# Performance work log

Measured on AMD Instinct MI355X. Metric: run time of the kernel, lower is better.

The kernel has to match this reference:

```python
import jax, jax.numpy as jnp
import numpy as np

N = 10000      # nodes per QA graph
E = 128000     # edges per QA graph
A = 5          # answers (multiple choice)
D = 300        # glove embedding dim
H = 8          # heads layer 1
C1 = 64        # per-head out channels layer 1 (concat -> 512)
HID = 512
NEG_SLOPE = 0.2
EPS = 1e-16


def gat_layer(x, edge_index, W, a_src, a_dst, bias, concat):
    # x: [N, Din]; edge_index: [2, E]; W: [Din, H*C]; a_src/a_dst: [H, C]
    Hh, C = a_src.shape
    h = (x @ W).reshape(N, Hh, C)                      # transformed node feats
    alpha_src = (h * a_src[None]).sum(-1)              # [N, H]
    alpha_dst = (h * a_dst[None]).sum(-1)              # [N, H]
    src, dst = edge_index[0], edge_index[1]
    e = jax.nn.leaky_relu(alpha_src[src] + alpha_dst[dst], NEG_SLOPE)  # [E, H]
    # edge softmax grouped by destination node
    m = jax.ops.segment_max(e, dst, num_segments=N)    # [N, H]
    ex = jnp.exp(e - m[dst])
    denom = jax.ops.segment_sum(ex, dst, num_segments=N)
    alpha = ex / (denom[dst] + EPS)                    # [E, H]
    msg = alpha[:, :, None] * h[src]                   # [E, H, C]
    out = jax.ops.segment_sum(msg, dst, num_segments=N)  # [N, H, C]
    out = out.reshape(N, Hh * C) if concat else out.mean(axis=1)
    return out + bias, alpha


def setup_inputs() -> dict:
    key = jax.random.key(0)
    ks = jax.random.split(key, 10)
    s = 0.05
    return {
        "x": jax.random.normal(ks[0], (A, N, D), jnp.float32),
        "edge_index": jax.random.randint(ks[1], (A, 2, E), 0, N, dtype=jnp.int32),
        "W1": jax.random.normal(ks[2], (D, H * C1), jnp.float32) * s,
        "att_src1": jax.random.normal(ks[3], (H, C1), jnp.float32) * s,
        "att_dst1": jax.random.normal(ks[4], (H, C1), jnp.float32) * s,
        "bias1": jnp.zeros((H * C1,), jnp.float32),
        "W2": jax.random.normal(ks[5], (HID, 1), jnp.float32) * s,
        "att_src2": jax.random.normal(ks[6], (1, 1), jnp.float32) * s,
        "att_dst2": jax.random.normal(ks[7], (1, 1), jnp.float32) * s,
        "bias2": jnp.zeros((1,), jnp.float32),
    }


def reference(x, edge_index, W1, att_src1, att_dst1, bias1, W2, att_src2, att_dst2, bias2):
    def per_answer(xa, ei):
        h1, _ = gat_layer(xa, ei, W1, att_src1, att_dst1, bias1, concat=True)
        h1 = jax.nn.relu(h1)
        h2, alpha = gat_layer(h1, ei, W2, att_src2, att_dst2, bias2, concat=False)
        proba = h2.mean()                                  # scalar (x.mean(dim=0))
        # aggregate_attention: attention[dst] += edge_weight (edge_additive)
        att = jax.ops.segment_sum(alpha[:, 0], ei[1], num_segments=N)
        return proba, att

    proba_vec, atts = jax.vmap(per_answer)(x, edge_index)  # [A], [A, N]
    sel = atts[jnp.argmax(proba_vec)]                      # attentions[argmax]
    return proba_vec, sel
```

## Files before the change

### kernel.cpp

```cpp
#include <hip/hip_runtime.h>
#include <hip/hip_bf16.h>
#include <math.h>

#define NN 10000
#define EE 128000
#define AA 5
#define DD 300
#define HH 8
#define CC 64
#define HC 512
#define MM (AA*NN)
#define KP 320
#define NT (KP / 32)
#define NBM ((MM + 63) / 64)
#define SCB 40
#define SCN 250

typedef __attribute__((ext_vector_type(8))) _Float16 f16x8;
typedef __attribute__((ext_vector_type(4))) float f32x4;
typedef __attribute__((ext_vector_type(2))) float f32x2;
typedef unsigned short ushort;
typedef unsigned char uchar;

__device__ __forceinline__ ushort f2bf(float f) {
    unsigned u = __float_as_uint(f);
    unsigned r = u + 0x7fffu + ((u >> 16) & 1u);
    return (ushort)(r >> 16);
}
__device__ __forceinline__ float bf2f(ushort h) {
    return __uint_as_float(((unsigned)h) << 16);
}


__global__ void zero_cnt(int* cnt) {
    int i = blockIdx.x * 256 + threadIdx.x;
    if (i < AA * NN) cnt[i] = 0;
}

__global__ void count_edges(const int* __restrict__ ei, int* __restrict__ cnt) {
    int a = blockIdx.y;
    int e = blockIdx.x * 256 + threadIdx.x;
    if (e < EE) {
        int dst = ei[(size_t)a * 2 * EE + EE + e];
        atomicAdd(&cnt[a * NN + dst], 1);
    }
}


__global__ __launch_bounds__(256) void scan_bsum(const int* __restrict__ cnt,
                                                 int* __restrict__ bsum) {
    int a = blockIdx.y, b = blockIdx.x;
    int l = threadIdx.x;
    int v = (l < SCN) ? cnt[a * NN + b * SCN + l] : 0;
    #pragma unroll
    for (int o = 1; o < 64; o <<= 1) v += __shfl_xor(v, o);
    __shared__ int red[4];
    if ((l & 63) == 0) red[l >> 6] = v;
    __syncthreads();
    if (l == 0) bsum[a * SCB + b] = red[0] + red[1] + red[2] + red[3];
}

__global__ __launch_bounds__(64) void scan_bscan(const int* __restrict__ bsum,
                                                 int* __restrict__ boff,
                                                 int* __restrict__ offs) {
    int a = blockIdx.x;
    int l = threadIdx.x;
    int v = (l < SCB) ? bsum[a * SCB + l] : 0;
    int sc = v;
    #pragma unroll
    for (int o = 1; o < 64; o <<= 1) {
        int u = __shfl_up(sc, o);
        if (l >= o) sc += u;
    }
    if (l < SCB) boff[a * SCB + l] = sc - v;
    if (l == 63) offs[a * (NN + 1) + NN] = sc;
}

__global__ __launch_bounds__(256) void scan_final(const int* __restrict__ cnt,
                                                  const int* __restrict__ boff,
                                                  int* __restrict__ offs,
                                                  int* __restrict__ cursor) {
    int a = blockIdx.y, b = blockIdx.x;
    int l = threadIdx.x;
    int i = b * SCN + l;
    int v = (l < SCN) ? cnt[a * NN + i] : 0;
    int sc = v;
    int lane = l & 63, wv = l >> 6;
    #pragma unroll
    for (int o = 1; o < 64; o <<= 1) {
        int u = __shfl_up(sc, o);
        if (lane >= o) sc += u;
    }
    __shared__ int ws[4];
    if (lane == 63) ws[wv] = sc;
    __syncthreads();
    int woff = 0;
    #pragma unroll
    for (int w = 0; w < 4; ++w) woff += (w < wv) ? ws[w] : 0;
    if (l < SCN) {
        int o = boff[a * SCB + b] + woff + sc - v;
        offs[a * (NN + 1) + i] = o;
        cursor[a * (NN + 1) + i] = o;
    }
}

__global__ void scatter_edges(const int* __restrict__ ei, int* __restrict__ cursor,
                              int* __restrict__ csr_eid) {
    int a = blockIdx.y;
    int e = blockIdx.x * 256 + threadIdx.x;
    if (e < EE) {
        int dst = ei[(size_t)a * 2 * EE + EE + e];
        int pos = atomicAdd(&cursor[a * (NN + 1) + dst], 1);
        csr_eid[(size_t)a * EE + pos] = e;
    }
}

__global__ __launch_bounds__(256) void sort_src(const int* __restrict__ ei,
                                                const int* __restrict__ offs,
                                                int* __restrict__ csr_eid,
                                                int* __restrict__ csr_src,
                                                int* __restrict__ csr_dst) {
    int a = blockIdx.y;
    int wid = threadIdx.x >> 6, l = threadIdx.x & 63;
    int n = blockIdx.x * 4 + wid;
    if (n >= NN) return;
    const int* offsA = offs + a * (NN + 1);
    int beg = offsA[n], end = offsA[n + 1];
    int deg = end - beg;
    int* seg = csr_eid + (size_t)a * EE + beg;
    const int* srcrow = ei + (size_t)a * 2 * EE;
    if (deg <= 64) {
        int v = (l < deg) ? seg[l] : 0x7fffffff;
        #pragma unroll
        for (int k = 2; k <= 64; k <<= 1)
            #pragma unroll
            for (int j = k >> 1; j > 0; j >>= 1) {
                int p = __shfl_xor(v, j);
                bool keepMin = (((l & k) == 0) == ((l & j) == 0));
                int mn = min(v, p), mx = max(v, p);
                v = keepMin ? mn : mx;
            }
        if (l < deg) {
            csr_src[(size_t)a * EE + beg + l] = srcrow[v];
            csr_dst[(size_t)a * EE + beg + l] = n;
        }
    } else {
        if (l == 0) {
            for (int i = 1; i < deg; ++i) {
                int key = seg[i];
                int j = i - 1;
                while (j >= 0 && seg[j] > key) { seg[j + 1] = seg[j]; --j; }
                seg[j + 1] = key;
            }
        }
        __builtin_amdgcn_wave_barrier();
        for (int i = l; i < deg; i += 64) {
            csr_src[(size_t)a * EE + beg + i] = srcrow[seg[i]];
            csr_dst[(size_t)a * EE + beg + i] = n;
        }
    }
}


__global__ __launch_bounds__(256) void pack_x(const float* __restrict__ X,
                                              ushort* __restrict__ Xp) {
    int gid = blockIdx.x * 256 + threadIdx.x;
    if (gid >= NBM * NT * 4 * 64) return;
    int l = gid & 63;
    int fr = (gid >> 6) & 3;
    int rest = gid >> 8;
    int ks = rest % NT;
    int bmi = rest / NT;
    int row = bmi * 64 + fr * 16 + (l & 15);
    int k = ks * 32 + (l >> 4) * 8;
    f16x8 o;
    if (row < MM && k + 8 <= DD) {
        float4 v0 = *(const float4*)(X + (size_t)row * DD + k);
        float4 v1 = *(const float4*)(X + (size_t)row * DD + k + 4);
        o[0] = (_Float16)v0.x; o[1] = (_Float16)v0.y;
        o[2] = (_Float16)v0.z; o[3] = (_Float16)v0.w;
        o[4] = (_Float16)v1.x; o[5] = (_Float16)v1.y;
        o[6] = (_Float16)v1.z; o[7] = (_Float16)v1.w;
    } else {
        #pragma unroll
        for (int j = 0; j < 8; ++j)
            o[j] = (row < MM && k + j < DD) ? (_Float16)X[(size_t)row * DD + k + j]
                                            : (_Float16)0.f;
    }
    *(f16x8*)(Xp + (size_t)gid * 8) = o;
}

__global__ __launch_bounds__(256) void pack_w(const float* __restrict__ W,
                                              ushort* __restrict__ Wp) {
    int gid = blockIdx.x * 256 + threadIdx.x;
    if (gid >= HH * NT * 4 * 64) return;
    int l = gid & 63;
    int fc = (gid >> 6) & 3;
    int rest = gid >> 8;
    int ks = rest % NT;
    int head = rest / NT;
    int col = head * 64 + fc * 16 + (l & 15);
    int k = ks * 32 + (l >> 4) * 8;
    f16x8 o;
    #pragma unroll
    for (int j = 0; j < 8; ++j)
        o[j] = (k + j < DD) ? (_Float16)W[(size_t)(k + j) * HC + col] : (_Float16)0.f;
    *(f16x8*)(Wp + (size_t)gid * 8) = o;
}


__global__ __launch_bounds__(256) void gemm_f16(const ushort* __restrict__ Xp,
                                                const ushort* __restrict__ Wp,
                                                const float* __restrict__ att_src1,
                                                const float* __restrict__ att_dst1,
                                                uchar* __restrict__ Hout,
                                                float* __restrict__ asrc,
                                                float* __restrict__ adst) {
    int wid = blockIdx.x * 4 + (threadIdx.x >> 6);
    int bmi = wid >> 3, head = wid & 7;
    if (bmi >= NBM) return;
    int bm = bmi * 64;
    int l = threadIdx.x & 63;
    int l16 = l & 15, kg = l >> 4;

    const ushort* Abase = Xp + (size_t)bmi * NT * 2048 + l * 8;
    const ushort* Bbase = Wp + (size_t)head * NT * 2048 + l * 8;

    f32x4 zz = {0.f, 0.f, 0.f, 0.f};
    f32x4 acc[4][4];
    #pragma unroll
    for (int i = 0; i < 4; ++i)
        #pragma unroll
        for (int j = 0; j < 4; ++j) acc[i][j] = zz;

    f16x8 aX[4], bX[4], aY[4], bY[4];
    #pragma unroll
    for (int f = 0; f < 4; ++f) {
        aX[f] = *(const f16x8*)(Abase + f * 512);
        bX[f] = *(const f16x8*)(Bbase + f * 512);
    }

    #pragma unroll
    for (int kk = 0; kk < NT; kk += 2) {
        if (kk + 1 < NT) {
            #pragma unroll
            for (int f = 0; f < 4; ++f) {
                aY[f] = *(const f16x8*)(Abase + (kk + 1) * 2048 + f * 512);
                bY[f] = *(const f16x8*)(Bbase + (kk + 1) * 2048 + f * 512);
            }
        }
        #pragma unroll
        for (int fr = 0; fr < 4; ++fr)
            #pragma unroll
            for (int fc = 0; fc < 4; ++fc)
                acc[fr][fc] = __builtin_amdgcn_mfma_f32_16x16x32_f16(aX[fr], bX[fc], acc[fr][fc], 0, 0, 0);
        if (kk + 2 < NT) {
            #pragma unroll
            for (int f = 0; f < 4; ++f) {
                aX[f] = *(const f16x8*)(Abase + (kk + 2) * 2048 + f * 512);
                bX[f] = *(const f16x8*)(Bbase + (kk + 2) * 2048 + f * 512);
            }
        }
        if (kk + 1 < NT) {
            #pragma unroll
            for (int fr = 0; fr < 4; ++fr)
                #pragma unroll
                for (int fc = 0; fc < 4; ++fc)
                    acc[fr][fc] = __builtin_amdgcn_mfma_f32_16x16x32_f16(aY[fr], bY[fc], acc[fr][fc], 0, 0, 0);
        }
    }

    float sv[4], dv[4];
    #pragma unroll
    for (int fc = 0; fc < 4; ++fc) {
        sv[fc] = att_src1[head * 64 + fc * 16 + l16];
        dv[fc] = att_dst1[head * 64 + fc * 16 + l16];
    }
    #pragma unroll
    for (int fr = 0; fr < 4; ++fr) {
        #pragma unroll
        for (int r = 0; r < 4; ++r) {
            int row = bm + fr * 16 + kg * 4 + r;
            bool ok = row < MM;
            float ps = 0.f, pd = 0.f;
            #pragma unroll
            for (int fc = 0; fc < 4; ++fc) {
                float val = acc[fr][fc][r];
                if (ok) {
                    int pk = __builtin_amdgcn_cvt_pk_fp8_f32(val, val, 0, false);
                    Hout[(size_t)row * HC + head * 64 + fc * 16 + l16] = (uchar)(pk & 0xff);
                }
                ps = fmaf(val, sv[fc], ps);
                pd = fmaf(val, dv[fc], pd);
            }
            #pragma unroll
            for (int o = 1; o < 16; o <<= 1) {
                ps += __shfl_xor(ps, o);
                pd += __shfl_xor(pd, o);
            }
            if (l16 == 0 && ok) {
                asrc[(size_t)row * HH + head] = ps;
                adst[(size_t)row * HH + head] = pd;
            }
        }
    }
}


__global__ __launch_bounds__(256) void edge_w(const int* __restrict__ csr_src,
                                              const int* __restrict__ csr_dst,
                                              const float* __restrict__ asrc,
                                              const float* __restrict__ adst,
                                              float* __restrict__ w4) {
    int a = blockIdx.y;
    int gid = blockIdx.x * 256 + threadIdx.x;
    if (gid >= EE * HH) return;
    int slot = gid >> 3, hd = gid & 7;
    int s = csr_src[(size_t)a * EE + slot];
    int d = csr_dst[(size_t)a * EE + slot];
    float v = asrc[((size_t)a * NN + s) * HH + hd] + adst[((size_t)a * NN + d) * HH + hd];
    v = v > 0.f ? v : 0.2f * v;
    w4[(((size_t)a * 2 + (hd >> 2)) * EE + slot) * 4 + (hd & 3)] = __expf(v);
}


__global__ __launch_bounds__(256) void layer1_agg(const uchar* __restrict__ h1,
                                                  const float* __restrict__ w4,
                                                  const int* __restrict__ offs,
                                                  const int* __restrict__ csr_src,
                                                  const float* __restrict__ bias1,
                                                  const float* __restrict__ W2,
                                                  float* __restrict__ h2p) {
    int a = blockIdx.y;
    int hf = blockIdx.z;
    int wid = threadIdx.x >> 6, l = threadIdx.x & 63;
    int n = blockIdx.x * 4 + wid;
    int l32 = l & 31;
    int ehalf = l >> 5;
    int hs = l32 >> 3;

    const int* offsA = offs + a * (NN + 1);
    int beg = offsA[n], end = offsA[n + 1];
    int deg = end - beg;
    const int* srcs = csr_src + (size_t)a * EE + beg;
    const float* wA = w4 + (((size_t)a * 2 + hf) * EE + beg) * 4;
    const uchar* h1A = h1 + (size_t)a * NN * HC + hf * 256;

    float denom = 0.f;
    float acc[8] = {};

    for (int c0 = 0; c0 < deg; c0 += 16) {
        int ei_w = c0 + (l >> 2);
        float w_reg = (ei_w < deg) ? wA[c0 * 4 + l] : 0.f;
        denom += w_reg;
        int s_reg = srcs[min(c0 + (l & 15), deg - 1)];
        #pragma unroll
        for (int j = 0; j < 16; j += 2) {
            int e = j + ehalf;
            float wj = __shfl(w_reg, e * 4 + hs);
            int sj = __shfl(s_reg, min(e, 15));
            const uchar* rp = h1A + (size_t)sj * HC + l32 * 8;
            uint2 hv = *(const uint2*)rp;
            f32x2 p0 = __builtin_amdgcn_cvt_pk_f32_fp8((int)hv.x, false);
            f32x2 p1 = __builtin_amdgcn_cvt_pk_f32_fp8((int)hv.x, true);
            f32x2 p2 = __builtin_amdgcn_cvt_pk_f32_fp8((int)hv.y, false);
            f32x2 p3 = __builtin_amdgcn_cvt_pk_f32_fp8((int)hv.y, true);
            acc[0] = fmaf(wj, p0[0], acc[0]);
            acc[1] = fmaf(wj, p0[1], acc[1]);
            acc[2] = fmaf(wj, p1[0], acc[2]);
            acc[3] = fmaf(wj, p1[1], acc[3]);
            acc[4] = fmaf(wj, p2[0], acc[4]);
            acc[5] = fmaf(wj, p2[1], acc[5]);
            acc[6] = fmaf(wj, p3[0], acc[6]);
            acc[7] = fmaf(wj, p3[1], acc[7]);
        }
    }
    #pragma unroll
    for (int k = 0; k < 8; ++k) acc[k] += __shfl_xor(acc[k], 32);
    #pragma unroll
    for (int o = 4; o < 64; o <<= 1) denom += __shfl_xor(denom, o);
    float dn = __shfl(denom, hs);
    float inv = 1.f / (dn + 1e-16f);

    int cb = hf * 256 + l32 * 8;
    float4 b0 = *(const float4*)(bias1 + cb);
    float4 b1 = *(const float4*)(bias1 + cb + 4);
    float4 w0 = *(const float4*)(W2 + cb);
    float4 w1 = *(const float4*)(W2 + cb + 4);
    float bz[8] = {b0.x, b0.y, b0.z, b0.w, b1.x, b1.y, b1.z, b1.w};
    float wz[8] = {w0.x, w0.y, w0.z, w0.w, w1.x, w1.y, w1.z, w1.w};
    float p = 0.f;
    #pragma unroll
    for (int k = 0; k < 8; ++k) {
        float z = fmaf(acc[k], inv, bz[k]);
        z = z > 0.f ? z : 0.f;
        p = fmaf(z, wz[k], p);
    }
    #pragma unroll
    for (int o = 1; o < 32; o <<= 1) p += __shfl_xor(p, o);
    if (l == 0) h2p[((size_t)hf * AA + a) * NN + n] = p;
}

__global__ void sum_h2(const float* __restrict__ h2p, float* __restrict__ h2) {
    int i = blockIdx.x * 256 + threadIdx.x;
    if (i < AA * NN) h2[i] = h2p[i] + h2p[(size_t)AA * NN + i];
}


#define L2GRID 40

__global__ __launch_bounds__(256) void layer2_proba(const float* __restrict__ h2,
                                                    const int* __restrict__ offs,
                                                    const int* __restrict__ csr_src,
                                                    const float* __restrict__ att_src2,
                                                    const float* __restrict__ att_dst2,
                                                    const float* __restrict__ bias2,
                                                    float* __restrict__ partials) {
    int a = blockIdx.y;
    int n = blockIdx.x * 256 + threadIdx.x;
    float out2 = 0.f;
    if (n < NN) {
        const int* offsA = offs + a * (NN + 1);
        const int* srcs = csr_src + (size_t)a * EE;
        const float* h2A = h2 + (size_t)a * NN;
        float as2 = att_src2[0], ad2 = att_dst2[0];
        int beg = offsA[n], end = offsA[n + 1];
        float adn = h2A[n] * ad2;
        float denom = 0.f, accv = 0.f;
        for (int i = beg; i < end; ++i) {
            float hs = h2A[srcs[i]];
            float v = fmaf(hs, as2, adn);
            v = v > 0.f ? v : 0.2f * v;
            float w = __expf(v);
            denom += w;
            accv = fmaf(w, hs, accv);
        }
        out2 = accv / (denom + 1e-16f) + bias2[0];
    }
    __shared__ float red[256];
    red[threadIdx.x] = out2;
    __syncthreads();
    for (int s = 128; s > 0; s >>= 1) {
        if (threadIdx.x < s) red[threadIdx.x] += red[threadIdx.x + s];
        __syncthreads();
    }
    if (threadIdx.x == 0) partials[a * L2GRID + blockIdx.x] = red[0];
}

__global__ __launch_bounds__(256) void finalize_proba(const float* __restrict__ partials,
                                                      float* __restrict__ out,
                                                      int* __restrict__ best) {
    int tid = threadIdx.x;
    __shared__ float red[256];
    red[tid] = (tid < AA * L2GRID) ? partials[tid] : 0.f;
    __syncthreads();
    if (tid == 0) {
        float pv[AA];
        for (int a = 0; a < AA; ++a) {
            float s = 0.f;
            for (int i = 0; i < L2GRID; ++i) s += red[a * L2GRID + i];
            pv[a] = s / (float)NN;
            out[a] = pv[a];
        }
        int b = 0;
        for (int a = 1; a < AA; ++a)
            if (pv[a] > pv[b]) b = a;
        *best = b;
    }
}

__global__ void write_sel(const int* __restrict__ cnt, const int* __restrict__ best,
                          float* __restrict__ out) {
    int n = blockIdx.x * 256 + threadIdx.x;
    if (n < NN) out[AA + n] = (cnt[(*best) * NN + n] > 0) ? 1.0f : 0.0f;
}


extern "C" void kernel_launch(void* const* d_in, const int* in_sizes, int n_in,
                              void* d_out, int out_size, void* d_ws, size_t ws_size,
                              hipStream_t stream) {
    const float* x        = (const float*)d_in[0];
    const int*   ei       = (const int*)d_in[1];
    const float* W1       = (const float*)d_in[2];
    const float* att_src1 = (const float*)d_in[3];
    const float* att_dst1 = (const float*)d_in[4];
    const float* bias1    = (const float*)d_in[5];
    const float* W2       = (const float*)d_in[6];
    const float* att_src2 = (const float*)d_in[7];
    const float* att_dst2 = (const float*)d_in[8];
    const float* bias2    = (const float*)d_in[9];
    float* out = (float*)d_out;

    char* ws = (char*)d_ws;
    size_t off = 0;
    auto alloc = [&](size_t bytes) {
        size_t cur = off;
        off += (bytes + 255) & ~(size_t)255;
        return cur;
    };
    uchar*  h1      = (uchar*)(ws + alloc(sizeof(uchar) * (size_t)MM * HC));
    ushort* xp      = (ushort*)(ws + alloc(sizeof(ushort) * (size_t)NBM * NT * 2048));
    float*  asrc    = (float*)(ws + alloc(sizeof(float) * (size_t)MM * HH));
    float*  adst    = (float*)(ws + alloc(sizeof(float) * (size_t)MM * HH));
    float*  h2      = (float*)(ws + alloc(sizeof(float) * (size_t)MM));
    float*  h2p     = (float*)(ws + alloc(sizeof(float) * 2 * (size_t)MM));
    int*    cnt     = (int*)(ws + alloc(sizeof(int) * (size_t)AA * NN));
    int*    offs    = (int*)(ws + alloc(sizeof(int) * (size_t)AA * (NN + 1)));
    int*    cursor  = (int*)(ws + alloc(sizeof(int) * (size_t)AA * (NN + 1)));
    int*    bsum    = (int*)(ws + alloc(sizeof(int) * (size_t)AA * SCB));
    int*    boff    = (int*)(ws + alloc(sizeof(int) * (size_t)AA * SCB));
    int*    csr_eid = (int*)(ws + alloc(sizeof(int) * (size_t)AA * EE));
    int*    csr_src = (int*)(ws + alloc(sizeof(int) * (size_t)AA * EE));
    int*    csr_dst = (int*)(ws + alloc(sizeof(int) * (size_t)AA * EE));
    float*  w4      = (float*)(ws + alloc(sizeof(float) * (size_t)AA * EE * HH));
    float*  partials= (float*)(ws + alloc(sizeof(float) * AA * L2GRID));
    int*    best    = (int*)(ws + alloc(sizeof(int) * 16));
    ushort* wp      = (ushort*)(ws + alloc(sizeof(ushort) * (size_t)HH * NT * 2048));
    (void)ws_size; (void)in_sizes; (void)n_in; (void)out_size;

    pack_w<<<dim3((HH * NT * 256 + 255) / 256), dim3(256), 0, stream>>>(W1, wp);
    pack_x<<<dim3((NBM * NT * 256 + 255) / 256), dim3(256), 0, stream>>>(x, xp);

    zero_cnt<<<dim3((AA * NN + 255) / 256), dim3(256), 0, stream>>>(cnt);
    count_edges<<<dim3(EE / 256, AA), dim3(256), 0, stream>>>(ei, cnt);
    scan_bsum<<<dim3(SCB, AA), dim3(256), 0, stream>>>(cnt, bsum);
    scan_bscan<<<dim3(AA), dim3(64), 0, stream>>>(bsum, boff, offs);
    scan_final<<<dim3(SCB, AA), dim3(256), 0, stream>>>(cnt, boff, offs, cursor);
    scatter_edges<<<dim3(EE / 256, AA), dim3(256), 0, stream>>>(ei, cursor, csr_eid);
    sort_src<<<dim3(NN / 4, AA), dim3(256), 0, stream>>>(ei, offs, csr_eid, csr_src, csr_dst);

    gemm_f16<<<dim3((NBM * 8 + 3) / 4), dim3(256), 0, stream>>>(
        xp, wp, att_src1, att_dst1, h1, asrc, adst);

    edge_w<<<dim3(EE * HH / 256, AA), dim3(256), 0, stream>>>(csr_src, csr_dst,
                                                              asrc, adst, w4);

    layer1_agg<<<dim3(NN / 4, AA, 2), dim3(256), 0, stream>>>(h1, w4, offs, csr_src,
                                                              bias1, W2, h2p);
    sum_h2<<<dim3((AA * NN + 255) / 256), dim3(256), 0, stream>>>(h2p, h2);

    layer2_proba<<<dim3(L2GRID, AA), dim3(256), 0, stream>>>(h2, offs, csr_src,
                                                             att_src2, att_dst2, bias2,
                                                             partials);

    finalize_proba<<<dim3(1), dim3(256), 0, stream>>>(partials, out, best);
    write_sel<<<dim3((NN + 255) / 256), dim3(256), 0, stream>>>(cnt, best, out);
}
```

Before: 244.0 us.

## Fuse edge weight computation into sort_src and merge layer1 aggregation halves

Moves the leaky-relu/exp edge-weight computation into the CSR sort kernel, which now runs after the GEMM. This removes the separate edge_w kernel and the csr_dst array. The layer-1 aggregation now handles all 512 channels per wavefront with 8 edges per step and prefetches the next batch of weights and sources. That removes the two-half grid and the sum_h2 reduction kernel. The trade-offs are less parallelism in aggregation and serialising the sort behind the GEMM.

```diff
diff --git a/kernel.cpp b/kernel.cpp
--- a/kernel.cpp
+++ b/kernel.cpp
@@ -30,6 +30,10 @@
 __device__ __forceinline__ float bf2f(ushort h) {
     return __uint_as_float(((unsigned)h) << 16);
 }
+__device__ __forceinline__ float leaky_exp(float v) {
+    v = v > 0.f ? v : 0.2f * v;
+    return __expf(v);
+}
 
 
 __global__ void zero_cnt(int* cnt) {
@@ -115,11 +119,14 @@
     }
 }
 
+
 __global__ __launch_bounds__(256) void sort_src(const int* __restrict__ ei,
                                                 const int* __restrict__ offs,
                                                 int* __restrict__ csr_eid,
                                                 int* __restrict__ csr_src,
-                                                int* __restrict__ csr_dst) {
+                                                const float* __restrict__ asrc,
+                                                const float* __restrict__ adst,
+                                                float* __restrict__ w_csr) {
     int a = blockIdx.y;
     int wid = threadIdx.x >> 6, l = threadIdx.x & 63;
     int n = blockIdx.x * 4 + wid;
@@ -129,6 +136,11 @@
     int deg = end - beg;
     int* seg = csr_eid + (size_t)a * EE + beg;
     const int* srcrow = ei + (size_t)a * 2 * EE;
+    const float* asrcA = asrc + (size_t)a * NN * HH;
+    const float* adstA = adst + (size_t)a * NN * HH;
+    float4 d0 = *(const float4*)(adstA + (size_t)n * HH);
+    float4 d1 = *(const float4*)(adstA + (size_t)n * HH + 4);
+
     if (deg <= 64) {
         int v = (l < deg) ? seg[l] : 0x7fffffff;
         #pragma unroll
@@ -141,8 +153,18 @@
                 v = keepMin ? mn : mx;
             }
         if (l < deg) {
-            csr_src[(size_t)a * EE + beg + l] = srcrow[v];
-            csr_dst[(size_t)a * EE + beg + l] = n;
+            int s = srcrow[v];
+            csr_src[(size_t)a * EE + beg + l] = s;
+            float4 s0 = *(const float4*)(asrcA + (size_t)s * HH);
+            float4 s1 = *(const float4*)(asrcA + (size_t)s * HH + 4);
+            float4 w0, w1;
+            w0.x = leaky_exp(s0.x + d0.x); w0.y = leaky_exp(s0.y + d0.y);
+            w0.z = leaky_exp(s0.z + d0.z); w0.w = leaky_exp(s0.w + d0.w);
+            w1.x = leaky_exp(s1.x + d1.x); w1.y = leaky_exp(s1.y + d1.y);
+            w1.z = leaky_exp(s1.z + d1.z); w1.w = leaky_exp(s1.w + d1.w);
+            float* wp = w_csr + ((size_t)a * EE + beg + l) * HH;
+            *(float4*)(wp) = w0;
+            *(float4*)(wp + 4) = w1;
         }
     } else {
         if (l == 0) {
@@ -155,8 +177,18 @@
         }
         __builtin_amdgcn_wave_barrier();
         for (int i = l; i < deg; i += 64) {
-            csr_src[(size_t)a * EE + beg + i] = srcrow[seg[i]];
-            csr_dst[(size_t)a * EE + beg + i] = n;
+            int s = srcrow[seg[i]];
+            csr_src[(size_t)a * EE + beg + i] = s;
+            float4 s0 = *(const float4*)(asrcA + (size_t)s * HH);
+            float4 s1 = *(const float4*)(asrcA + (size_t)s * HH + 4);
+            float4 w0, w1;
+            w0.x = leaky_exp(s0.x + d0.x); w0.y = leaky_exp(s0.y + d0.y);
+            w0.z = leaky_exp(s0.z + d0.z); w0.w = leaky_exp(s0.w + d0.w);
+            w1.x = leaky_exp(s1.x + d1.x); w1.y = leaky_exp(s1.y + d1.y);
+            w1.z = leaky_exp(s1.z + d1.z); w1.w = leaky_exp(s1.w + d1.w);
+            float* wp = w_csr + ((size_t)a * EE + beg + i) * HH;
+            *(float4*)(wp) = w0;
+            *(float4*)(wp + 4) = w1;
         }
     }
 }
@@ -307,82 +339,69 @@
 }
 
 
-__global__ __launch_bounds__(256) void edge_w(const int* __restrict__ csr_src,
-                                              const int* __restrict__ csr_dst,
-                                              const float* __restrict__ asrc,
-                                              const float* __restrict__ adst,
-                                              float* __restrict__ w4) {
-    int a = blockIdx.y;
-    int gid = blockIdx.x * 256 + threadIdx.x;
-    if (gid >= EE * HH) return;
-    int slot = gid >> 3, hd = gid & 7;
-    int s = csr_src[(size_t)a * EE + slot];
-    int d = csr_dst[(size_t)a * EE + slot];
-    float v = asrc[((size_t)a * NN + s) * HH + hd] + adst[((size_t)a * NN + d) * HH + hd];
-    v = v > 0.f ? v : 0.2f * v;
-    w4[(((size_t)a * 2 + (hd >> 2)) * EE + slot) * 4 + (hd & 3)] = __expf(v);
-}
-
-
 __global__ __launch_bounds__(256) void layer1_agg(const uchar* __restrict__ h1,
-                                                  const float* __restrict__ w4,
+                                                  const float* __restrict__ w_csr,
                                                   const int* __restrict__ offs,
                                                   const int* __restrict__ csr_src,
                                                   const float* __restrict__ bias1,
                                                   const float* __restrict__ W2,
-                                                  float* __restrict__ h2p) {
+                                                  float* __restrict__ h2) {
     int a = blockIdx.y;
-    int hf = blockIdx.z;
     int wid = threadIdx.x >> 6, l = threadIdx.x & 63;
     int n = blockIdx.x * 4 + wid;
-    int l32 = l & 31;
-    int ehalf = l >> 5;
-    int hs = l32 >> 3;
+    int eg = l >> 3;
+    int gh = l >> 3;
 
     const int* offsA = offs + a * (NN + 1);
     int beg = offsA[n], end = offsA[n + 1];
     int deg = end - beg;
     const int* srcs = csr_src + (size_t)a * EE + beg;
-    const float* wA = w4 + (((size_t)a * 2 + hf) * EE + beg) * 4;
-    const uchar* h1A = h1 + (size_t)a * NN * HC + hf * 256;
+    const float* wA = w_csr + ((size_t)a * EE + beg) * HH;
+    const uchar* h1A = h1 + (size_t)a * NN * HC;
 
     float denom = 0.f;
     float acc[8] = {};
 
-    for (int c0 = 0; c0 < deg; c0 += 16) {
-        int ei_w = c0 + (l >> 2);
-        float w_reg = (ei_w < deg) ? wA[c0 * 4 + l] : 0.f;
-        denom += w_reg;
-        int s_reg = srcs[min(c0 + (l & 15), deg - 1)];
+    float w_cur = (eg < deg) ? wA[l] : 0.f;
+    int s_cur = (eg < deg) ? srcs[eg] : 0;
+
+    for (int c0 = 0; c0 < deg; c0 += 8) {
+        float w_nxt = 0.f;
+        int s_nxt = 0;
+        if (c0 + 8 + eg < deg) {
+            w_nxt = wA[(c0 + 8) * 8 + l];
+            s_nxt = srcs[c0 + 8 + eg];
+        }
         #pragma unroll
-        for (int j = 0; j < 16; j += 2) {
-            int e = j + ehalf;
-            float wj = __shfl(w_reg, e * 4 + hs);
-            int sj = __shfl(s_reg, min(e, 15));
-            const uchar* rp = h1A + (size_t)sj * HC + l32 * 8;
-            uint2 hv = *(const uint2*)rp;
-            f32x2 p0 = __builtin_amdgcn_cvt_pk_f32_fp8((int)hv.x, false);
-            f32x2 p1 = __builtin_amdgcn_cvt_pk_f32_fp8((int)hv.x, true);
-            f32x2 p2 = __builtin_amdgcn_cvt_pk_f32_fp8((int)hv.y, false);
-            f32x2 p3 = __builtin_amdgcn_cvt_pk_f32_fp8((int)hv.y, true);
-            acc[0] = fmaf(wj, p0[0], acc[0]);
-            acc[1] = fmaf(wj, p0[1], acc[1]);
-            acc[2] = fmaf(wj, p1[0], acc[2]);
-            acc[3] = fmaf(wj, p1[1], acc[3]);
-            acc[4] = fmaf(wj, p2[0], acc[4]);
-            acc[5] = fmaf(wj, p2[1], acc[5]);
-            acc[6] = fmaf(wj, p3[0], acc[6]);
-            acc[7] = fmaf(wj, p3[1], acc[7]);
-        }
-    }
-    #pragma unroll
-    for (int k = 0; k < 8; ++k) acc[k] += __shfl_xor(acc[k], 32);
-    #pragma unroll
-    for (int o = 4; o < 64; o <<= 1) denom += __shfl_xor(denom, o);
-    float dn = __shfl(denom, hs);
+        for (int j = 0; j < 8; ++j) {
+            if (c0 + j < deg) {
+                float wj = __shfl(w_cur, j * 8 + gh);
+                int sj = __shfl(s_cur, j * 8);
+                uint2 hv = *(const uint2*)(h1A + (size_t)sj * HC + (l << 3));
+                f32x2 p0 = __builtin_amdgcn_cvt_pk_f32_fp8((int)hv.x, false);
+                f32x2 p1 = __builtin_amdgcn_cvt_pk_f32_fp8((int)hv.x, true);
+                f32x2 p2 = __builtin_amdgcn_cvt_pk_f32_fp8((int)hv.y, false);
+                f32x2 p3 = __builtin_amdgcn_cvt_pk_f32_fp8((int)hv.y, true);
+                acc[0] = fmaf(wj, p0[0], acc[0]);
+                acc[1] = fmaf(wj, p0[1], acc[1]);
+                acc[2] = fmaf(wj, p1[0], acc[2]);
+                acc[3] = fmaf(wj, p1[1], acc[3]);
+                acc[4] = fmaf(wj, p2[0], acc[4]);
+                acc[5] = fmaf(wj, p2[1], acc[5]);
+                acc[6] = fmaf(wj, p3[0], acc[6]);
+                acc[7] = fmaf(wj, p3[1], acc[7]);
+            }
+        }
+        denom += w_cur;
+        w_cur = w_nxt;
+        s_cur = s_nxt;
+    }
+    #pragma unroll
+    for (int o = 8; o < 64; o <<= 1) denom += __shfl_xor(denom, o);
+    float dn = __shfl(denom, gh);
     float inv = 1.f / (dn + 1e-16f);
 
-    int cb = hf * 256 + l32 * 8;
+    int cb = l * 8;
     float4 b0 = *(const float4*)(bias1 + cb);
     float4 b1 = *(const float4*)(bias1 + cb + 4);
     float4 w0 = *(const float4*)(W2 + cb);
@@ -397,13 +416,8 @@
         p = fmaf(z, wz[k], p);
     }
     #pragma unroll
-    for (int o = 1; o < 32; o <<= 1) p += __shfl_xor(p, o);
-    if (l == 0) h2p[((size_t)hf * AA + a) * NN + n] = p;
-}
-
-__global__ void sum_h2(const float* __restrict__ h2p, float* __restrict__ h2) {
-    int i = blockIdx.x * 256 + threadIdx.x;
-    if (i < AA * NN) h2[i] = h2p[i] + h2p[(size_t)AA * NN + i];
+    for (int o = 1; o < 64; o <<= 1) p += __shfl_xor(p, o);
+    if (l == 0) h2[(size_t)a * NN + n] = p;
 }
 
 
@@ -503,7 +517,6 @@
     float*  asrc    = (float*)(ws + alloc(sizeof(float) * (size_t)MM * HH));
     float*  adst    = (float*)(ws + alloc(sizeof(float) * (size_t)MM * HH));
     float*  h2      = (float*)(ws + alloc(sizeof(float) * (size_t)MM));
-    float*  h2p     = (float*)(ws + alloc(sizeof(float) * 2 * (size_t)MM));
     int*    cnt     = (int*)(ws + alloc(sizeof(int) * (size_t)AA * NN));
     int*    offs    = (int*)(ws + alloc(sizeof(int) * (size_t)AA * (NN + 1)));
     int*    cursor  = (int*)(ws + alloc(sizeof(int) * (size_t)AA * (NN + 1)));
@@ -511,8 +524,7 @@
     int*    boff    = (int*)(ws + alloc(sizeof(int) * (size_t)AA * SCB));
     int*    csr_eid = (int*)(ws + alloc(sizeof(int) * (size_t)AA * EE));
     int*    csr_src = (int*)(ws + alloc(sizeof(int) * (size_t)AA * EE));
-    int*    csr_dst = (int*)(ws + alloc(sizeof(int) * (size_t)AA * EE));
-    float*  w4      = (float*)(ws + alloc(sizeof(float) * (size_t)AA * EE * HH));
+    float*  w_csr   = (float*)(ws + alloc(sizeof(float) * (size_t)AA * EE * HH));
     float*  partials= (float*)(ws + alloc(sizeof(float) * AA * L2GRID));
     int*    best    = (int*)(ws + alloc(sizeof(int) * 16));
     ushort* wp      = (ushort*)(ws + alloc(sizeof(ushort) * (size_t)HH * NT * 2048));
@@ -527,17 +539,15 @@
     scan_bscan<<<dim3(AA), dim3(64), 0, stream>>>(bsum, boff, offs);
     scan_final<<<dim3(SCB, AA), dim3(256), 0, stream>>>(cnt, boff, offs, cursor);
     scatter_edges<<<dim3(EE / 256, AA), dim3(256), 0, stream>>>(ei, cursor, csr_eid);
-    sort_src<<<dim3(NN / 4, AA), dim3(256), 0, stream>>>(ei, offs, csr_eid, csr_src, csr_dst);
 
     gemm_f16<<<dim3((NBM * 8 + 3) / 4), dim3(256), 0, stream>>>(
         xp, wp, att_src1, att_dst1, h1, asrc, adst);
 
-    edge_w<<<dim3(EE * HH / 256, AA), dim3(256), 0, stream>>>(csr_src, csr_dst,
-                                                              asrc, adst, w4);
-
-    layer1_agg<<<dim3(NN / 4, AA, 2), dim3(256), 0, stream>>>(h1, w4, offs, csr_src,
-                                                              bias1, W2, h2p);
-    sum_h2<<<dim3((AA * NN + 255) / 256), dim3(256), 0, stream>>>(h2p, h2);
+    sort_src<<<dim3(NN / 4, AA), dim3(256), 0, stream>>>(ei, offs, csr_eid, csr_src,
+                                                         asrc, adst, w_csr);
+
+    layer1_agg<<<dim3(NN / 4, AA), dim3(256), 0, stream>>>(h1, w_csr, offs, csr_src,
+                                                           bias1, W2, h2);
 
     layer2_proba<<<dim3(L2GRID, AA), dim3(256), 0, stream>>>(h2, offs, csr_src,
                                                              att_src2, att_dst2, bias2,
```

After: 235.6 us. 3.4% less time.
